# Kernel optimization log

Measured on AMD Instinct MI355X. Metric: run time of the kernel, lower is better.

## Reference

```python
import jax, jax.numpy as jnp
import numpy as np

# region/recall params from layer config
NUM_CLASSES = 20
NUM_ANCHORS = 5
ANCHORS = jnp.array([[1.3221, 1.73145], [3.19275, 4.00944], [5.05587, 8.09892],
                     [9.47112, 4.84053], [11.2364, 10.0071]], dtype=jnp.float32)
CONF_THRESH = 0.5
NMS_THRESH = 0.45
IOU_THRESH = 0.5
EPS = 1e-6


def setup_inputs() -> dict:
    key = jax.random.key(0)
    k1, k2 = jax.random.split(key)
    output = jax.random.normal(k1, (8, NUM_ANCHORS * (5 + NUM_CLASSES), 19, 19), dtype=jnp.float32)
    target = jax.random.uniform(k2, (8, 250), dtype=jnp.float32)  # [B, 50*5] rows: cls,cx,cy,w,h
    return {"output": output, "target": target}


def decode_region_boxes(output):
    """get_region_boxes: anchor decode. output [B, A*(5+C), H, W] -> boxes [B, A*H*W, 4] cxcywh (normalized), det_conf [B, A*H*W]."""
    B, _, H, W = output.shape
    o = output.reshape(B, NUM_ANCHORS, 5 + NUM_CLASSES, H, W)
    gx = jnp.arange(W, dtype=output.dtype)
    gy = jnp.arange(H, dtype=output.dtype)
    cx = (jax.nn.sigmoid(o[:, :, 0]) + gx[None, None, None, :]) / W
    cy = (jax.nn.sigmoid(o[:, :, 1]) + gy[None, None, :, None]) / H
    bw = jnp.exp(o[:, :, 2]) * (ANCHORS[:, 0] / W)[None, :, None, None]
    bh = jnp.exp(o[:, :, 3]) * (ANCHORS[:, 1] / H)[None, :, None, None]
    det_conf = jax.nn.sigmoid(o[:, :, 4])
    boxes = jnp.stack([cx, cy, bw, bh], axis=-1).reshape(B, -1, 4)
    return boxes, det_conf.reshape(B, -1)


def pairwise_iou(a, b):
    """bbox_iou(x1y1x2y2=False) for all pairs. a [..., Na, 4], b [..., Nb, 4] cxcywh -> [..., Na, Nb]."""
    ax1 = (a[..., 0] - a[..., 2] * 0.5)[..., :, None]
    ax2 = (a[..., 0] + a[..., 2] * 0.5)[..., :, None]
    ay1 = (a[..., 1] - a[..., 3] * 0.5)[..., :, None]
    ay2 = (a[..., 1] + a[..., 3] * 0.5)[..., :, None]
    bx1 = (b[..., 0] - b[..., 2] * 0.5)[..., None, :]
    bx2 = (b[..., 0] + b[..., 2] * 0.5)[..., None, :]
    by1 = (b[..., 1] - b[..., 3] * 0.5)[..., None, :]
    by2 = (b[..., 1] + b[..., 3] * 0.5)[..., None, :]
    uw = jnp.maximum(ax2, bx2) - jnp.minimum(ax1, bx1)
    uh = jnp.maximum(ay2, by2) - jnp.minimum(ay1, by1)
    aw = a[..., 2][..., :, None]; ah = a[..., 3][..., :, None]
    bw = b[..., 2][..., None, :]; bh = b[..., 3][..., None, :]
    cw = aw + bw - uw
    ch = ah + bh - uh
    carea = jnp.where((cw > 0) & (ch > 0), cw * ch, 0.0)
    uarea = aw * ah + bw * bh - carea
    return carea / uarea


def greedy_nms_keep(iou_mat, valid):
    """Sequential greedy NMS over conf-sorted boxes using precomputed IoU. iou_mat [N,N], valid [N] bool."""
    N = valid.shape[0]
    idx = jnp.arange(N)
    def body(i, keep):
        sup = keep[i] & (iou_mat[i] > NMS_THRESH) & (idx > i)
        return keep & (~sup)
    return jax.lax.fori_loop(0, N, body, valid)


def reference(output, target):
    B = output.shape[0]
    boxes, det = decode_region_boxes(output)              # [B,N,4], [B,N]
    # sort by det_conf descending (nms sort order)
    order = jnp.argsort(-det, axis=1)
    boxes = jnp.take_along_axis(boxes, order[..., None], axis=1)
    det = jnp.take_along_axis(det, order, axis=1)
    valid = det > CONF_THRESH                             # boxes that enter nms (conf filter in get_region_boxes)
    iou_mat = pairwise_iou(boxes, boxes)                  # [B,N,N]
    keep = jax.vmap(greedy_nms_keep)(iou_mat, valid)      # [B,N]
    proposals = jnp.sum(keep)
    # ground truth: [B,T,5] rows [cls,cx,cy,w,h]; num_gts = boxes until first cx==0
    truths = target.reshape(B, -1, 5)
    gt_valid = jnp.cumprod((truths[..., 1] != 0).astype(jnp.int32), axis=1).astype(bool)  # [B,T]
    total = jnp.sum(gt_valid)
    iou_gt = pairwise_iou(truths[..., 1:5], boxes)        # [B,T,N]
    best_iou = jnp.max(jnp.where(keep[:, None, :], iou_gt, 0.0), axis=-1)  # [B,T]
    correct = jnp.sum(gt_valid & (best_iou > IOU_THRESH))
    total_f = total.astype(jnp.float32)
    prop_f = proposals.astype(jnp.float32)
    corr_f = correct.astype(jnp.float32)
    precision = corr_f / (prop_f + EPS)
    recall = corr_f / (total_f + EPS)
    fscore = 2.0 * precision * recall / (precision + recall + EPS)
    return jnp.stack([total_f, prop_f, corr_f, precision, recall, fscore])
```

## Files before the change

### kernel.cpp

```cpp
#include <hip/hip_runtime.h>

namespace {
constexpr int NA    = 5;
constexpr int NCELL = 361;
constexpr int NBOX  = 1805;
constexpr int NBOXP = 1856;
constexpr int NT1   = 1024;
constexpr int TMAX  = 50;
constexpr float CONF_T = 0.5f;
constexpr float NMS_T  = 0.45f;
constexpr float IOU_T  = 0.5f;
constexpr int NWMAX   = 32;
constexpr int ROWPAD  = 1856;
constexpr int SOA_STRIDE = NBOXP;
constexpr int SOA_ARR    = 8 * SOA_STRIDE;
constexpr size_t WS_COUNT = 0;
constexpr size_t WS_M     = 64;
constexpr size_t WS_SOA   = 256;
constexpr size_t WS_SUP   = 360448;
}

__device__ __constant__ float d_anchw[NA] = {1.3221f, 3.19275f, 5.05587f, 9.47112f, 11.2364f};
__device__ __constant__ float d_anchh[NA] = {1.73145f, 4.00944f, 8.09892f, 4.84053f, 10.0071f};

__device__ inline unsigned long long shflx64(unsigned long long v, int m) {
    int lo = __shfl_xor((int)(unsigned)(v & 0xffffffffull), m, 64);
    int hi = __shfl_xor((int)(unsigned)(v >> 32), m, 64);
    return ((unsigned long long)(unsigned)hi << 32) | (unsigned)lo;
}
__device__ inline unsigned long long rdlane64(unsigned long long v, int l) {
    unsigned lo = (unsigned)__builtin_amdgcn_readlane((int)(unsigned)(v & 0xffffffffull), l);
    unsigned hi = (unsigned)__builtin_amdgcn_readlane((int)(unsigned)(v >> 32), l);
    return ((unsigned long long)hi << 32) | lo;
}
__device__ inline void barrier_lgkm() {
    __asm__ volatile("" ::: "memory");
    __builtin_amdgcn_s_waitcnt(0xC07F);
    __builtin_amdgcn_s_barrier();
    __asm__ volatile("" ::: "memory");
}

__global__ __launch_bounds__(NT1, 1) void k_decode_sort(
    const float* __restrict__ net, float* __restrict__ soa,
    int* __restrict__ Marr, int* __restrict__ counters)
{
    __shared__ unsigned long long skey[2048];
    __shared__ float4 sbox[NBOX];
    __shared__ int sCnt;
    const int b = blockIdx.x, tid = threadIdx.x, lane = tid & 63;
    const float* op = net + (size_t)b * (NA * 25 * NCELL);
    if (tid == 0) sCnt = 0;
    if (b == 0 && tid < 4) counters[tid] = 0;
    __syncthreads();

    for (int n = tid; n < NBOX; n += NT1) {
        int a = n / NCELL;
        int r = n - a * NCELL;
        int y = r / 19;
        int x = r - y * 19;
        int base = a * 25 * NCELL + r;
        float t0 = op[base];
        float t1 = op[base + 1 * NCELL];
        float t2 = op[base + 2 * NCELL];
        float t3 = op[base + 3 * NCELL];
        float t4 = op[base + 4 * NCELL];
        float cx = (1.0f / (1.0f + expf(-t0)) + (float)x) / 19.0f;
        float cy = (1.0f / (1.0f + expf(-t1)) + (float)y) / 19.0f;
        float bw = expf(t2) * (d_anchw[a] / 19.0f);
        float bh = expf(t3) * (d_anchh[a] / 19.0f);
        float det = 1.0f / (1.0f + expf(-t4));
        sbox[n] = make_float4(cx, cy, bw, bh);
        bool valid = det > CONF_T;
        unsigned long long bm = __ballot(valid);
        int base0 = 0;
        if (lane == 0 && bm) base0 = atomicAdd(&sCnt, __popcll(bm));
        base0 = __shfl(base0, 0, 64);
        if (valid) {
            int pos = base0 + __popcll(bm & ((1ull << lane) - 1ull));
            skey[pos] = ((unsigned long long)(~__float_as_uint(det)) << 32) | (unsigned)n;
        }
    }
    __syncthreads();
    const int M = sCnt;
    int S = 64; while (S < M) S <<= 1;
    for (int n = M + tid; n < S; n += NT1) skey[n] = ~0ull;
    __syncthreads();

    unsigned long long v[8];
    const int nt8 = S >> 3;
    const int base8 = tid << 3;
    auto cas = [&](int xx, int yy, bool up) {
        unsigned long long a = v[xx], c = v[yy];
        if ((a > c) == up) { v[xx] = c; v[yy] = a; }
    };
    if (tid < nt8) {
        #pragma unroll
        for (int p = 0; p < 8; ++p) v[p] = skey[base8 + p];
        cas(0,1,true); cas(2,3,false); cas(4,5,true); cas(6,7,false);
        cas(0,2,true); cas(1,3,true); cas(4,6,false); cas(5,7,false);
        cas(0,1,true); cas(2,3,true); cas(4,5,false); cas(6,7,false);
        bool u8 = ((base8 & 8) == 0);
        cas(0,4,u8); cas(1,5,u8); cas(2,6,u8); cas(3,7,u8);
        cas(0,2,u8); cas(1,3,u8); cas(4,6,u8); cas(5,7,u8);
        cas(0,1,u8); cas(2,3,u8); cas(4,5,u8); cas(6,7,u8);
        #pragma unroll
        for (int p = 0; p < 8; ++p) skey[base8 + p] = v[p];
    }
    __syncthreads();
    for (unsigned k = 16; k <= (unsigned)S; k <<= 1) {
        for (unsigned j = k >> 1; j >= 8; j >>= 1) {
            for (unsigned m = tid; m < (unsigned)(S >> 1); m += NT1) {
                unsigned i = ((m & ~(j - 1)) << 1) | (m & (j - 1));
                unsigned p = i | j;
                bool up = ((i & k) == 0);
                unsigned long long a = skey[i], c2 = skey[p];
                if ((a > c2) == up) { skey[i] = c2; skey[p] = a; }
            }
            __syncthreads();
        }
        if (tid < nt8) {
            #pragma unroll
            for (int p = 0; p < 8; ++p) v[p] = skey[base8 + p];
            bool up = ((base8 & k) == 0);
            cas(0,4,up); cas(1,5,up); cas(2,6,up); cas(3,7,up);
            cas(0,2,up); cas(1,3,up); cas(4,6,up); cas(5,7,up);
            cas(0,1,up); cas(2,3,up); cas(4,5,up); cas(6,7,up);
            #pragma unroll
            for (int p = 0; p < 8; ++p) skey[base8 + p] = v[p];
        }
        __syncthreads();
    }

    float* X1 = soa + 0 * SOA_ARR + b * SOA_STRIDE;
    float* Y1 = soa + 1 * SOA_ARR + b * SOA_STRIDE;
    float* X2 = soa + 2 * SOA_ARR + b * SOA_STRIDE;
    float* Y2 = soa + 3 * SOA_ARR + b * SOA_STRIDE;
    float* Wd = soa + 4 * SOA_ARR + b * SOA_STRIDE;
    float* Hd = soa + 5 * SOA_ARR + b * SOA_STRIDE;
    const int mceil = (M + 63) & ~63;
    for (int p = tid; p < mceil; p += NT1) {
        float4 bx = make_float4(0.f, 0.f, 0.f, 0.f);
        if (p < M) bx = sbox[(unsigned)(skey[p] & 0xffffffffull)];
        X1[p] = bx.x - 0.5f * bx.z;
        Y1[p] = bx.y - 0.5f * bx.w;
        X2[p] = bx.x + 0.5f * bx.z;
        Y2[p] = bx.y + 0.5f * bx.w;
        Wd[p] = bx.z;
        Hd[p] = bx.w;
    }
    if (tid == 0) Marr[b] = M;
}

__global__ __launch_bounds__(256) void k_iou_maskT(
    const float* __restrict__ soa, const int* __restrict__ Marr,
    unsigned long long* __restrict__ supT)
{
    const int blk  = blockIdx.x;
    const int b    = blk & 7;
    const int g    = blk >> 3;
    const int wv   = threadIdx.x >> 6;
    const int lane = threadIdx.x & 63;
    const int M = Marr[b];
    const int i0 = g * 16 + wv * 4;
    if (i0 >= M) return;
    const float* X1 = soa + 0 * SOA_ARR + b * SOA_STRIDE;
    const float* Y1 = soa + 1 * SOA_ARR + b * SOA_STRIDE;
    const float* X2 = soa + 2 * SOA_ARR + b * SOA_STRIDE;
    const float* Y2 = soa + 3 * SOA_ARR + b * SOA_STRIDE;
    const float* Wd = soa + 4 * SOA_ARR + b * SOA_STRIDE;
    const float* Hd = soa + 5 * SOA_ARR + b * SOA_STRIDE;
    const int nch = (M + 63) >> 6;
    const int w0  = i0 >> 6;

    float ax1[4], ay1[4], ax2[4], ay2[4], aw[4], ah[4], aarea[4];
    #pragma unroll
    for (int r = 0; r < 4; ++r) {
        int ir = i0 + r; if (ir >= M) ir = M - 1;
        ax1[r] = X1[ir]; ay1[r] = Y1[ir];
        ax2[r] = X2[ir]; ay2[r] = Y2[ir];
        aw[r]  = Wd[ir]; ah[r]  = Hd[ir];
        aarea[r] = aw[r] * ah[r];
    }
    unsigned long long myw0 = 0, myw1 = 0, myw2 = 0, myw3 = 0;
    for (int w = w0; w < nch; ++w) {
        int j = (w << 6) + lane;
        float bx1 = X1[j], by1 = Y1[j];
        float bx2 = X2[j], by2 = Y2[j];
        float bw  = Wd[j], bh  = Hd[j];
        float barea = bw * bh;
        bool jok = (j < M);
        #pragma unroll
        for (int r = 0; r < 4; ++r) {
            bool pred = false;
            if (jok && j > i0 + r) {
                float uw = fmaxf(ax2[r], bx2) - fminf(ax1[r], bx1);
                float uh = fmaxf(ay2[r], by2) - fminf(ay1[r], by1);
                float cw = aw[r] + bw - uw;
                float ch = ah[r] + bh - uh;
                if (cw > 0.0f && ch > 0.0f) {
                    float ca = cw * ch;
                    float ua = aarea[r] + barea - ca;
                    pred = ca > NMS_T * ua;
                }
            }
            unsigned long long m = __ballot(pred);
            if (w == lane) {
                if      (r == 0) myw0 = m;
                else if (r == 1) myw1 = m;
                else if (r == 2) myw2 = m;
                else             myw3 = m;
            }
        }
    }
    if (lane >= w0 && lane < nch) {
        unsigned long long* dst = supT + ((size_t)b * 32 + lane) * ROWPAD;
        dst[i0] = myw0;
        if (i0 + 1 < M) dst[i0 + 1] = myw1;
        if (i0 + 2 < M) dst[i0 + 2] = myw2;
        if (i0 + 3 < M) dst[i0 + 3] = myw3;
    }
}

__global__ __launch_bounds__(1024, 1) void k_sweep(
    const float* __restrict__ soa, const float* __restrict__ tgt,
    const int* __restrict__ Marr, const unsigned long long* __restrict__ supT,
    int* __restrict__ counters, float* __restrict__ out)
{
    __shared__ float X1s[NBOXP], Y1s[NBOXP], X2s[NBOXP], Y2s[NBOXP];
    __shared__ float Wss[NBOXP], Hss[NBOXP];
    __shared__ unsigned long long rmw[NWMAX], keepw[NWMAX];
    __shared__ int sNV, sCorr, sProp;
    const int b = blockIdx.x, tid = threadIdx.x;
    const int wv = tid >> 6, lane = tid & 63;
    const int M = Marr[b];
    const int nwa = (M + 63) >> 6;
    const unsigned long long* sb = supT + (size_t)b * 32 * ROWPAD;

    if (tid < NWMAX) { rmw[tid] = 0ull; keepw[tid] = 0ull; }
    if (tid == 0) { sCorr = 0; sProp = 0; }

    {
        int mceil = (M + 63) & ~63;
        const float* X1 = soa + 0 * SOA_ARR + b * SOA_STRIDE;
        const float* Y1 = soa + 1 * SOA_ARR + b * SOA_STRIDE;
        const float* X2 = soa + 2 * SOA_ARR + b * SOA_STRIDE;
        const float* Y2 = soa + 3 * SOA_ARR + b * SOA_STRIDE;
        const float* Wd = soa + 4 * SOA_ARR + b * SOA_STRIDE;
        const float* Hd = soa + 5 * SOA_ARR + b * SOA_STRIDE;
        for (int p = tid; p < mceil; p += 1024) {
            X1s[p] = X1[p]; Y1s[p] = Y1[p];
            X2s[p] = X2[p]; Y2s[p] = Y2[p];
            Wss[p] = Wd[p]; Hss[p] = Hd[p];
        }
    }
    if (wv == 2) {
        float cxv = (lane < TMAX) ? tgt[b * 250 + lane * 5 + 1] : 0.0f;
        unsigned long long bm = __ballot(cxv != 0.0f);
        unsigned long long inv = (~bm) & ((1ull << TMAX) - 1ull);
        if (lane == 0) sNV = inv ? (__ffsll((long long)inv) - 1) : TMAX;
    }

    const int w1 = (wv >= 1) ? wv : -1;
    const int w2 = (wv >= 1 && wv + 15 <= 28) ? (wv + 15) : -1;
    unsigned long long cur1 = 0, cur2 = 0, diag = 0;
    if (wv == 0 && nwa > 0) diag = sb[lane];
    if (w1 >= 1 && w1 < nwa) cur1 = sb[(size_t)w1 * ROWPAD + lane];
    if (w2 >= 1 && w2 < nwa) cur2 = sb[(size_t)w2 * ROWPAD + lane];
    __syncthreads();

    for (int t = 0; t < nwa; ++t) {
        if (wv == 0) {
            unsigned long long cur = rmw[t];
            int rem = M - (t << 6);
            unsigned long long vm = (rem >= 64) ? ~0ull : ((1ull << rem) - 1ull);
            unsigned long long live = vm & ~cur;
            while (live) {
                int i = __ffsll((long long)live) - 1;
                unsigned long long w64 = rdlane64(diag, i);
                cur |= w64;
                live &= ~w64;
                live &= ~(1ull << i);
            }
            unsigned long long kp = vm & ~cur;
            if (lane == 0) keepw[t] = kp;
            int tn = t + 1;
            if (tn < nwa) diag = sb[(size_t)tn * ROWPAD + (tn << 6) + lane];
        }
        barrier_lgkm();
        {
            unsigned long long kmt = keepw[t];
            if (w1 > t && w1 < nwa) {
                unsigned long long c = ((kmt >> lane) & 1ull) ? cur1 : 0ull;
                c |= shflx64(c, 1);  c |= shflx64(c, 2);  c |= shflx64(c, 4);
                c |= shflx64(c, 8);  c |= shflx64(c, 16); c |= shflx64(c, 32);
                if (lane == 0) rmw[w1] |= c;
            }
            if (w2 > t && w2 < nwa) {
                unsigned long long c = ((kmt >> lane) & 1ull) ? cur2 : 0ull;
                c |= shflx64(c, 1);  c |= shflx64(c, 2);  c |= shflx64(c, 4);
                c |= shflx64(c, 8);  c |= shflx64(c, 16); c |= shflx64(c, 32);
                if (lane == 0) rmw[w2] |= c;
            }
            if (w1 > t + 1 && w1 < nwa) cur1 = sb[(size_t)w1 * ROWPAD + ((t + 1) << 6) + lane];
            if (w2 > t + 1 && w2 < nwa) cur2 = sb[(size_t)w2 * ROWPAD + ((t + 1) << 6) + lane];
        }
        barrier_lgkm();
    }

    if (wv == 0) {
        unsigned long long kv = (lane < NWMAX) ? keepw[lane] : 0ull;
        int pc = __popcll(kv);
        for (int d = 32; d > 0; d >>= 1) pc += __shfl_down(pc, d, 64);
        if (lane == 0) sProp = pc;
    }

    const int nv = sNV;
    for (int t = wv; t < nv; t += 16) {
        const float* g = tgt + b * 250 + t * 5;
        float gcx = g[1], gcy = g[2], gw = g[3], gh = g[4];
        float gx1 = gcx - 0.5f * gw, gx2 = gcx + 0.5f * gw;
        float gy1 = gcy - 0.5f * gh, gy2 = gcy + 0.5f * gh;
        float garea = gw * gh;
        float best = 0.0f;
        for (int j0 = 0; j0 < M; j0 += 64) {
            unsigned long long kw = keepw[j0 >> 6];
            if (kw == 0ull) continue;
            int j = j0 + lane;
            bool ok = (j < M) && ((kw >> lane) & 1ull);
            int js = (j < NBOXP) ? j : (NBOXP - 1);
            float bw = Wss[js], bh = Hss[js];
            float uw = fmaxf(gx2, X2s[js]) - fminf(gx1, X1s[js]);
            float uh = fmaxf(gy2, Y2s[js]) - fminf(gy1, Y1s[js]);
            float cww = gw + bw - uw, chh = gh + bh - uh;
            float ca = (cww > 0.0f && chh > 0.0f) ? cww * chh : 0.0f;
            float ua = garea + bw * bh - ca;
            float iou = ca / ua;
            best = fmaxf(best, ok ? iou : 0.0f);
        }
        for (int d = 32; d > 0; d >>= 1) best = fmaxf(best, __shfl_down(best, d, 64));
        if (lane == 0 && best > IOU_T) atomicAdd(&sCorr, 1);
    }
    barrier_lgkm();

    if (tid == 0) {
        atomicAdd(counters + 0, sProp);
        atomicAdd(counters + 1, sCorr);
        atomicAdd(counters + 2, sNV);
        __threadfence();
        int done = atomicAdd(counters + 3, 1);
        if (done == 7) {
            float prop  = (float)atomicAdd(counters + 0, 0);
            float corr  = (float)atomicAdd(counters + 1, 0);
            float total = (float)atomicAdd(counters + 2, 0);
            float prec = corr / (prop + 1e-6f);
            float rec  = corr / (total + 1e-6f);
            float fs   = 2.0f * prec * rec / (prec + rec + 1e-6f);
            out[0] = total;
            out[1] = prop;
            out[2] = corr;
            out[3] = prec;
            out[4] = rec;
            out[5] = fs;
        }
    }
}

extern "C" void kernel_launch(void* const* d_in, const int* in_sizes, int n_in,
                              void* d_out, int out_size, void* d_ws, size_t ws_size,
                              hipStream_t stream) {
    const float* net = (const float*)d_in[0];
    const float* tgt = (const float*)d_in[1];
    char* ws = (char*)d_ws;
    int* counters = (int*)(ws + WS_COUNT);
    int* Marr     = (int*)(ws + WS_M);
    float* soa    = (float*)(ws + WS_SOA);
    unsigned long long* supT = (unsigned long long*)(ws + WS_SUP);

    k_decode_sort<<<8, NT1, 0, stream>>>(net, soa, Marr, counters);
    int rowblocks = (NBOX + 15) / 16;
    k_iou_maskT<<<rowblocks * 8, 256, 0, stream>>>(soa, Marr, supT);
    k_sweep<<<8, 1024, 0, stream>>>(soa, tgt, Marr, supT, counters, (float*)d_out);
}
```

Baseline: 130.0 us.

## Pack suppression matrix triangularly and replace shuffle OR-reduction with LDS atomics

The transposed suppression bitmask storage changes from padded full rows per word-column to a packed lower-triangular layout, so only the needed entries are stored and read. In the sweep kernel, the per-wave 6-step 64-bit xor-shuffle OR reduction is replaced by per-lane 32-bit atomicOr into shared memory, done only by lanes whose box was kept and whose mask word is nonzero. This shortens the serial critical path between barriers in the greedy NMS sweep. The cost is possible LDS atomic contention when many lanes are kept.

```diff
diff --git a/kernel.cpp b/kernel.cpp
--- a/kernel.cpp
+++ b/kernel.cpp
@@ -10,24 +10,21 @@
 constexpr float CONF_T = 0.5f;
 constexpr float NMS_T  = 0.45f;
 constexpr float IOU_T  = 0.5f;
-constexpr int NWMAX   = 32;
-constexpr int ROWPAD  = 1856;
+constexpr int NW     = 29;
+constexpr int NWMAX  = 32;
 constexpr int SOA_STRIDE = NBOXP;
 constexpr int SOA_ARR    = 8 * SOA_STRIDE;
+constexpr int TRIW = 64 * (NW * (NW + 1) / 2);
 constexpr size_t WS_COUNT = 0;
 constexpr size_t WS_M     = 64;
 constexpr size_t WS_SOA   = 256;
 constexpr size_t WS_SUP   = 360448;
+__device__ inline size_t tri_off(int w) { return (size_t)32 * w * (w + 1); }
 }
 
 __device__ __constant__ float d_anchw[NA] = {1.3221f, 3.19275f, 5.05587f, 9.47112f, 11.2364f};
 __device__ __constant__ float d_anchh[NA] = {1.73145f, 4.00944f, 8.09892f, 4.84053f, 10.0071f};
 
-__device__ inline unsigned long long shflx64(unsigned long long v, int m) {
-    int lo = __shfl_xor((int)(unsigned)(v & 0xffffffffull), m, 64);
-    int hi = __shfl_xor((int)(unsigned)(v >> 32), m, 64);
-    return ((unsigned long long)(unsigned)hi << 32) | (unsigned)lo;
-}
 __device__ inline unsigned long long rdlane64(unsigned long long v, int l) {
     unsigned lo = (unsigned)__builtin_amdgcn_readlane((int)(unsigned)(v & 0xffffffffull), l);
     unsigned hi = (unsigned)__builtin_amdgcn_readlane((int)(unsigned)(v >> 32), l);
@@ -213,7 +210,7 @@
         }
     }
     if (lane >= w0 && lane < nch) {
-        unsigned long long* dst = supT + ((size_t)b * 32 + lane) * ROWPAD;
+        unsigned long long* dst = supT + (size_t)b * TRIW + tri_off(lane);
         dst[i0] = myw0;
         if (i0 + 1 < M) dst[i0 + 1] = myw1;
         if (i0 + 2 < M) dst[i0 + 2] = myw2;
@@ -228,15 +225,17 @@
 {
     __shared__ float X1s[NBOXP], Y1s[NBOXP], X2s[NBOXP], Y2s[NBOXP];
     __shared__ float Wss[NBOXP], Hss[NBOXP];
-    __shared__ unsigned long long rmw[NWMAX], keepw[NWMAX];
+    __shared__ unsigned rmwU[2 * NWMAX];
+    __shared__ unsigned long long keepw[NWMAX];
     __shared__ int sNV, sCorr, sProp;
     const int b = blockIdx.x, tid = threadIdx.x;
     const int wv = tid >> 6, lane = tid & 63;
     const int M = Marr[b];
     const int nwa = (M + 63) >> 6;
-    const unsigned long long* sb = supT + (size_t)b * 32 * ROWPAD;
-
-    if (tid < NWMAX) { rmw[tid] = 0ull; keepw[tid] = 0ull; }
+    const unsigned long long* sb = supT + (size_t)b * TRIW;
+
+    if (tid < 2 * NWMAX) rmwU[tid] = 0u;
+    if (tid < NWMAX) keepw[tid] = 0ull;
     if (tid == 0) { sCorr = 0; sProp = 0; }
 
     {
@@ -263,14 +262,15 @@
     const int w1 = (wv >= 1) ? wv : -1;
     const int w2 = (wv >= 1 && wv + 15 <= 28) ? (wv + 15) : -1;
     unsigned long long cur1 = 0, cur2 = 0, diag = 0;
-    if (wv == 0 && nwa > 0) diag = sb[lane];
-    if (w1 >= 1 && w1 < nwa) cur1 = sb[(size_t)w1 * ROWPAD + lane];
-    if (w2 >= 1 && w2 < nwa) cur2 = sb[(size_t)w2 * ROWPAD + lane];
+    if (wv == 0 && nwa > 0) diag = sb[tri_off(0) + lane];
+    if (w1 >= 1 && w1 < nwa) cur1 = sb[tri_off(w1) + lane];
+    if (w2 >= 1 && w2 < nwa) cur2 = sb[tri_off(w2) + lane];
     __syncthreads();
 
     for (int t = 0; t < nwa; ++t) {
         if (wv == 0) {
-            unsigned long long cur = rmw[t];
+            unsigned long long cur =
+                ((unsigned long long)rmwU[2 * t + 1] << 32) | rmwU[2 * t];
             int rem = M - (t << 6);
             unsigned long long vm = (rem >= 64) ? ~0ull : ((1ull << rem) - 1ull);
             unsigned long long live = vm & ~cur;
@@ -284,25 +284,24 @@
             unsigned long long kp = vm & ~cur;
             if (lane == 0) keepw[t] = kp;
             int tn = t + 1;
-            if (tn < nwa) diag = sb[(size_t)tn * ROWPAD + (tn << 6) + lane];
+            if (tn < nwa) diag = sb[tri_off(tn) + (tn << 6) + lane];
         }
         barrier_lgkm();
         {
             unsigned long long kmt = keepw[t];
-            if (w1 > t && w1 < nwa) {
-                unsigned long long c = ((kmt >> lane) & 1ull) ? cur1 : 0ull;
-                c |= shflx64(c, 1);  c |= shflx64(c, 2);  c |= shflx64(c, 4);
-                c |= shflx64(c, 8);  c |= shflx64(c, 16); c |= shflx64(c, 32);
-                if (lane == 0) rmw[w1] |= c;
-            }
-            if (w2 > t && w2 < nwa) {
-                unsigned long long c = ((kmt >> lane) & 1ull) ? cur2 : 0ull;
-                c |= shflx64(c, 1);  c |= shflx64(c, 2);  c |= shflx64(c, 4);
-                c |= shflx64(c, 8);  c |= shflx64(c, 16); c |= shflx64(c, 32);
-                if (lane == 0) rmw[w2] |= c;
-            }
-            if (w1 > t + 1 && w1 < nwa) cur1 = sb[(size_t)w1 * ROWPAD + ((t + 1) << 6) + lane];
-            if (w2 > t + 1 && w2 < nwa) cur2 = sb[(size_t)w2 * ROWPAD + ((t + 1) << 6) + lane];
+            bool kept = (kmt >> lane) & 1ull;
+            if (w1 > t && w1 < nwa && kept) {
+                unsigned lo = (unsigned)cur1, hi = (unsigned)(cur1 >> 32);
+                if (lo) atomicOr(&rmwU[2 * w1], lo);
+                if (hi) atomicOr(&rmwU[2 * w1 + 1], hi);
+            }
+            if (w2 > t && w2 < nwa && kept) {
+                unsigned lo = (unsigned)cur2, hi = (unsigned)(cur2 >> 32);
+                if (lo) atomicOr(&rmwU[2 * w2], lo);
+                if (hi) atomicOr(&rmwU[2 * w2 + 1], hi);
+            }
+            if (w1 > t + 1 && w1 < nwa) cur1 = sb[tri_off(w1) + ((t + 1) << 6) + lane];
+            if (w2 > t + 1 && w2 < nwa) cur2 = sb[tri_off(w2) + ((t + 1) << 6) + lane];
         }
         barrier_lgkm();
     }
```

Result: no change. 128.7 us (-1.1%).
